# Kernel optimization log

Hardware: AMD Instinct MI355X
Metric: run time of the kernel (lower is better)

Reference implementation:

```python
import jax, jax.numpy as jnp
import numpy as np

N = 4096          # nodes
F_IN = 1386       # txt_feat_len
NHID = 1024       # per-head hidden
NHEADS = 8
CODE = 64         # code_len
LRELU_ALPHA = 0.2
NEG_INF = -9e15


def _build_adj(x):
    # F.normalize + cosine sim, threshold 0.8, sign -> {0,1}, then symmetric D^-1/2 A D^-1/2
    norm = jnp.maximum(jnp.linalg.norm(x, axis=1, keepdims=True), 1e-12)
    xn = x / norm
    sim = xn @ xn.T                                  # (N,N)
    A = (sim >= 0.8).astype(x.dtype)                 # sign after thresholding
    rowsum = A.sum(axis=1)
    r = jnp.where(rowsum > 0, rowsum ** -0.5, 0.0)
    adj = r[:, None] * A * r[None, :]                # symmetric normalized
    return jax.lax.stop_gradient(adj)                # torch code detaches x / adj is non-diff


def _gat_head(x, W, a, adj, concat):
    # x: (N,Fin), W: (Fin,H), a: (2H,1)
    H = W.shape[1]
    Wh = x @ W                                        # (N,H)
    f1 = Wh @ a[:H]                                   # (N,1)
    f2 = Wh @ a[H:]                                   # (N,1)
    e = jax.nn.leaky_relu(f1 + f2.T, LRELU_ALPHA)     # (N,N) pairwise scores
    e = jnp.where(adj > 0, e, NEG_INF)
    att = jax.nn.softmax(e, axis=1)                   # masked softmax (dropout off: eval)
    h = att @ Wh                                      # (N,H)
    return jax.nn.elu(h) if concat else h


def setup_inputs() -> dict:
    key = jax.random.key(0)
    k = jax.random.split(key, 5)
    x = jax.random.normal(k[0], (N, F_IN), dtype=jnp.float32)
    s_in = 1.0 / np.sqrt(F_IN)
    W_att = jax.random.uniform(k[1], (NHEADS, F_IN, NHID), jnp.float32, -s_in, s_in)
    a_att = jax.random.uniform(k[2], (NHEADS, 2 * NHID, 1), jnp.float32, -0.1, 0.1)
    s_h = 1.0 / np.sqrt(NHEADS * NHID)
    W_out = jax.random.uniform(k[3], (NHEADS * NHID, CODE), jnp.float32, -s_h, s_h)
    a_out = jax.random.uniform(k[4], (2 * CODE, 1), jnp.float32, -0.1, 0.1)
    return {"x": x, "W_att": W_att, "a_att": a_att, "W_out": W_out, "a_out": a_out}


def reference(x, W_att, a_att, W_out, a_out):
    adj = _build_adj(x)
    # 8 concat heads, vmapped over the head axis
    heads = jax.vmap(lambda W, a: _gat_head(x, W, a, adj, True))(W_att, a_att)  # (8,N,NHID)
    h = jnp.transpose(heads, (1, 0, 2)).reshape(N, NHEADS * NHID)               # cat dim=1
    out = _gat_head(h, W_out, a_out, adj, False)                                # (N,CODE)
    code = jnp.tanh(1.0 * out)                                                   # alpha=1.0
    return code
```

## Files before the change

kernel.cpp:

```cpp
#include <hip/hip_runtime.h>
#include <hip/hip_bf16.h>
#include <stdint.h>
#include <math.h>


typedef __bf16 bf16x8 __attribute__((ext_vector_type(8)));
typedef float  f32x4  __attribute__((ext_vector_type(4)));
typedef unsigned short ushort8 __attribute__((ext_vector_type(8)));

#define AS1C(p) ((const __attribute__((address_space(1))) void*)(p))
#define AS3(p)  ((__attribute__((address_space(3))) void*)(p))

#define MODE_BF16 0
#define MODE_SIM  1
#define MODE_F32  2

__device__ __forceinline__ float bfbits2f(unsigned short u) {
    return __uint_as_float(((unsigned)u) << 16);
}
__device__ __forceinline__ unsigned short f2bfbits(float v) {
    __hip_bfloat16 b = __float2bfloat16(v);
    return *(unsigned short*)&b;
}

template<int MODE>
__global__ __launch_bounds__(256, 2)
void gemm_bt(const __hip_bfloat16* __restrict__ A,
             const __hip_bfloat16* __restrict__ B,
             int lda, int ldb, int K,
             void* __restrict__ Cv, int ldc, int Nreal,
             const float* __restrict__ norms,
             unsigned* __restrict__ mask,
             unsigned* __restrict__ summary,
             const float* __restrict__ a_att,
             float2* __restrict__ f12,
             int head_base,
             long long zA, long long zB, long long zC)
{
    __shared__ __align__(16) __hip_bfloat16 As[128 * 32];
    __shared__ __align__(16) __hip_bfloat16 Bs[128 * 32];

    const int tid  = threadIdx.x;
    const int lane = tid & 63;
    const int wave = tid >> 6;
    const int z    = blockIdx.z;

    int bx, by;
    if (MODE == MODE_SIM) {
        const int id = blockIdx.x;
        int t = (int)((sqrtf(8.f * id + 1.f) - 1.f) * 0.5f);
        while (t * (t + 1) / 2 > id) --t;
        while ((t + 1) * (t + 2) / 2 <= id) ++t;
        by = t; bx = id - t * (t + 1) / 2;
    } else {
        bx = blockIdx.x; by = blockIdx.y;
    }
    const int m0 = bx * 128;
    const int n0 = by * 128;

    A += (long long)z * zA;
    B += (long long)z * zB;

    f32x4 acc[4][4];
#pragma unroll
    for (int i = 0; i < 4; ++i)
#pragma unroll
        for (int j = 0; j < 4; ++j)
#pragma unroll
            for (int k = 0; k < 4; ++k) acc[i][j][k] = 0.f;

    const int wm = wave >> 1, wn = wave & 1;
    const int q  = lane >> 4, ln = lane & 15;

    const int kIters = K >> 5;
    for (int kt = 0; kt < kIters; ++kt) {
        __syncthreads();
#pragma unroll
        for (int p = 0; p < 2; ++p) {
            const int t   = p * 256 + tid;
            const int row = t >> 2;
            const int kb  = (t & 3) ^ ((t >> 3) & 3);
            const __hip_bfloat16* ga = A + (long long)(m0 + row) * lda + kt * 32 + kb * 8;
            const __hip_bfloat16* gb = B + (long long)(n0 + row) * ldb + kt * 32 + kb * 8;
            __hip_bfloat16* sa = As + (p * 256 + wave * 64) * 8;
            __hip_bfloat16* sb = Bs + (p * 256 + wave * 64) * 8;
            __builtin_amdgcn_global_load_lds(AS1C(ga), AS3(sa), 16, 0, 0);
            __builtin_amdgcn_global_load_lds(AS1C(gb), AS3(sb), 16, 0, 0);
        }
        __syncthreads();

        bf16x8 afr[4], bfr[4];
#pragma unroll
        for (int rg = 0; rg < 4; ++rg) {
            const int r = wm * 64 + rg * 16 + ln;
            const int s = q ^ ((r >> 1) & 3);
            afr[rg] = *(const bf16x8*)(As + r * 32 + s * 8);
        }
#pragma unroll
        for (int cg = 0; cg < 4; ++cg) {
            const int r = wn * 64 + cg * 16 + ln;
            const int s = q ^ ((r >> 1) & 3);
            bfr[cg] = *(const bf16x8*)(Bs + r * 32 + s * 8);
        }
#pragma unroll
        for (int rg = 0; rg < 4; ++rg)
#pragma unroll
            for (int cg = 0; cg < 4; ++cg)
                acc[rg][cg] = __builtin_amdgcn_mfma_f32_16x16x32_bf16(
                    afr[rg], bfr[cg], acc[rg][cg], 0, 0, 0);
    }

    const float* a1 = nullptr; const float* a2 = nullptr;
    if (MODE == MODE_BF16) {
        a1 = a_att + (long long)(head_base + z) * 2048;
        a2 = a1 + 1024;
    }
#pragma unroll
    for (int rg = 0; rg < 4; ++rg) {
#pragma unroll
        for (int i = 0; i < 4; ++i) {
            const int row = m0 + wm * 64 + rg * 16 + q * 4 + i;
            float s1 = 0.f, s2 = 0.f;
#pragma unroll
            for (int cg = 0; cg < 4; ++cg) {
                const int col = n0 + wn * 64 + cg * 16 + ln;
                const float v = acc[rg][cg][i];
                if (MODE == MODE_BF16) {
                    __hip_bfloat16* C = (__hip_bfloat16*)Cv + (long long)z * zC;
                    C[(long long)row * ldc + col] = __float2bfloat16(v);
                    s1 += v * a1[col];
                    s2 += v * a2[col];
                } else if (MODE == MODE_SIM) {
                    if (v >= 0.8f * norms[row] * norms[col]) {
                        atomicOr(&mask[row * 128 + (col >> 5)], 1u << (col & 31));
                        atomicOr(&summary[row * 4 + (col >> 10)], 1u << ((col >> 5) & 31));
                        atomicOr(&mask[col * 128 + (row >> 5)], 1u << (row & 31));
                        atomicOr(&summary[col * 4 + (row >> 10)], 1u << ((row >> 5) & 31));
                    }
                } else {
                    if (col < Nreal) {
                        float* C = (float*)Cv + (long long)z * zC;
                        C[(long long)row * ldc + col] = v;
                    }
                }
            }
            if (MODE == MODE_BF16) {
#pragma unroll
                for (int off = 8; off; off >>= 1) {
                    s1 += __shfl_down(s1, off, 16);
                    s2 += __shfl_down(s2, off, 16);
                }
                if (ln == 0) {
                    float2* fp = f12 + (long long)(head_base + z) * 4096 + row;
                    atomicAdd(&fp->x, s1);
                    atomicAdd(&fp->y, s2);
                }
            }
        }
    }
}

__global__ void convert_x(const float* __restrict__ x,
                          __hip_bfloat16* __restrict__ xb,
                          float* __restrict__ norms)
{
    const int i = blockIdx.x, tid = threadIdx.x;
    float ss = 0.f;
    for (int c = tid; c < 1408; c += 256) {
        float v = (c < 1386) ? x[(long long)i * 1386 + c] : 0.f;
        xb[(long long)i * 1408 + c] = __float2bfloat16(v);
        ss += v * v;
    }
    for (int off = 32; off; off >>= 1) ss += __shfl_down(ss, off);
    __shared__ float red[4];
    if ((tid & 63) == 0) red[tid >> 6] = ss;
    __syncthreads();
    if (tid == 0) norms[i] = fmaxf(sqrtf(red[0] + red[1] + red[2] + red[3]), 1e-12f);
}

__global__ void transpose_bf(const float* __restrict__ src,
                             __hip_bfloat16* __restrict__ dst,
                             int K, int N, int Kpad, int Npad,
                             long long sStride, long long dStride)
{
    __shared__ float ts[32][33];
    const int b  = blockIdx.z;
    const int k0 = blockIdx.x * 32;
    const int n0 = blockIdx.y * 32;
    const int tx = threadIdx.x, ty = threadIdx.y;
    const float* s = src + b * sStride;
    __hip_bfloat16* d = dst + b * dStride;
#pragma unroll
    for (int i = 0; i < 4; ++i) {
        const int k = k0 + ty + i * 8;
        const int n = n0 + tx;
        ts[ty + i * 8][tx] = (k < K && n < N) ? s[(long long)k * N + n] : 0.f;
    }
    __syncthreads();
#pragma unroll
    for (int i = 0; i < 4; ++i) {
        const int n  = n0 + ty + i * 8;
        const int kk = k0 + tx;
        if (n < Npad && kk < Kpad)
            d[(long long)n * Kpad + kk] = __float2bfloat16(ts[tx][ty + i * 8]);
    }
}

__global__ __launch_bounds__(256)
void attn_head(const __hip_bfloat16* __restrict__ Wh,
               const float2* __restrict__ f12,
               const unsigned* __restrict__ mask,
               const unsigned* __restrict__ summary,
               __hip_bfloat16* __restrict__ hout,
               int head_base, int BH)
{
    const int wv   = threadIdx.x >> 6;
    const int lane = threadIdx.x & 63;
    const int i    = blockIdx.x * 4 + wv;
    const int hl   = blockIdx.y;
    const int h    = head_base + hl;
    const float2* f = f12 + (long long)h * 4096;
    const float f1 = f[i].x;
    const unsigned* mrow = mask + (long long)i * 128;
    const __hip_bfloat16* WhH = Wh + (long long)hl * 4096 * 1024;
    const uint4 sm = *(const uint4*)(summary + (long long)i * 4);
    unsigned sw[4] = { sm.x, sm.y, sm.z, sm.w };
    const int cbase = lane * 16;

    float m = -INFINITY, l = 0.f;
    float acc[16];
#pragma unroll
    for (int k = 0; k < 16; ++k) acc[k] = 0.f;

#pragma unroll
    for (int s = 0; s < 4; ++s) {
        unsigned sb = sw[s];
        while (sb) {
            const int w = s * 32 + __builtin_ctz(sb);
            sb &= sb - 1;
            unsigned bits = mrow[w];
            while (bits) {
                const int j = w * 32 + __builtin_ctz(bits);
                bits &= bits - 1;
                float e = f1 + f[j].y;
                e = e > 0.f ? e : 0.2f * e;
                float wgt;
                if (e > m) {
                    const float sc = __expf(m - e);
                    l *= sc;
#pragma unroll
                    for (int k = 0; k < 16; ++k) acc[k] *= sc;
                    m = e; wgt = 1.f;
                } else {
                    wgt = __expf(e - m);
                }
                l += wgt;
                const ushort8* p = (const ushort8*)(WhH + (long long)j * 1024 + cbase);
                const ushort8 w0 = p[0], w1 = p[1];
#pragma unroll
                for (int k = 0; k < 8; ++k) acc[k]     += wgt * bfbits2f(w0[k]);
#pragma unroll
                for (int k = 0; k < 8; ++k) acc[k + 8] += wgt * bfbits2f(w1[k]);
            }
        }
    }
    const float inv = 1.f / l;
    ushort8 o0, o1;
#pragma unroll
    for (int k = 0; k < 8; ++k) {
        float v = acc[k] * inv;     v = v > 0.f ? v : (__expf(v) - 1.f); o0[k] = f2bfbits(v);
        float u = acc[k + 8] * inv; u = u > 0.f ? u : (__expf(u) - 1.f); o1[k] = f2bfbits(u);
    }
    ushort8* op = (ushort8*)(hout + (long long)i * (BH * 1024) + (long long)hl * 1024 + cbase);
    op[0] = o0; op[1] = o1;
}

__global__ void out_reduce_f(const float* __restrict__ parts,
                             const float* __restrict__ a_out,
                             float* __restrict__ Cout,
                             float* __restrict__ f1o,
                             float* __restrict__ f2o)
{
    const int i = blockIdx.x, c = threadIdx.x;
    float v = 0.f;
#pragma unroll
    for (int z = 0; z < 16; ++z) v += parts[(long long)z * 4096 * 64 + (long long)i * 64 + c];
    Cout[(long long)i * 64 + c] = v;
    float s1 = v * a_out[c];
    float s2 = v * a_out[64 + c];
    for (int off = 32; off; off >>= 1) { s1 += __shfl_down(s1, off); s2 += __shfl_down(s2, off); }
    if (c == 0) { f1o[i] = s1; f2o[i] = s2; }
}

__global__ __launch_bounds__(256)
void attn_out(const float* __restrict__ Cout,
              const float* __restrict__ f1o,
              const float* __restrict__ f2o,
              const unsigned* __restrict__ mask,
              const unsigned* __restrict__ summary,
              float* __restrict__ out)
{
    const int wv = threadIdx.x >> 6;
    const int c  = threadIdx.x & 63;
    const int i  = blockIdx.x * 4 + wv;
    const float f1 = f1o[i];
    const unsigned* mrow = mask + (long long)i * 128;
    const uint4 sm = *(const uint4*)(summary + (long long)i * 4);
    unsigned sw[4] = { sm.x, sm.y, sm.z, sm.w };
    float m = -INFINITY, l = 0.f, acc = 0.f;
#pragma unroll
    for (int s = 0; s < 4; ++s) {
        unsigned sb = sw[s];
        while (sb) {
            const int w = s * 32 + __builtin_ctz(sb);
            sb &= sb - 1;
            unsigned bits = mrow[w];
            while (bits) {
                const int j = w * 32 + __builtin_ctz(bits);
                bits &= bits - 1;
                float e = f1 + f2o[j];
                e = e > 0.f ? e : 0.2f * e;
                float wgt;
                if (e > m) { const float sc = __expf(m - e); l *= sc; acc *= sc; m = e; wgt = 1.f; }
                else       { wgt = __expf(e - m); }
                l += wgt;
                acc += wgt * Cout[(long long)j * 64 + c];
            }
        }
    }
    out[(long long)i * 64 + c] = tanhf(acc / l);
}

extern "C" void kernel_launch(void* const* d_in, const int* in_sizes, int n_in,
                              void* d_out, int out_size, void* d_ws, size_t ws_size,
                              hipStream_t stream)
{
    (void)in_sizes; (void)n_in; (void)out_size;
    const float* x     = (const float*)d_in[0];
    const float* W_att = (const float*)d_in[1];
    const float* a_att = (const float*)d_in[2];
    const float* W_out = (const float*)d_in[3];
    const float* a_out = (const float*)d_in[4];
    float* out = (float*)d_out;

    char* ws = (char*)d_ws;
    size_t off = 0;
    auto alloc = [&](size_t bytes) -> void* {
        void* p = ws + off;
        off += (bytes + 255) & ~(size_t)255;
        return p;
    };

    __hip_bfloat16* x_bf  = (__hip_bfloat16*)alloc(4096LL * 1408 * 2);
    __hip_bfloat16* Wt_bf = (__hip_bfloat16*)alloc(8LL * 1024 * 1408 * 2);
    __hip_bfloat16* WoutT = (__hip_bfloat16*)alloc(128LL * 8192 * 2);
    float*          norms = (float*)alloc(4096 * 4);
    unsigned*       mask  = (unsigned*)alloc(4096LL * 128 * 4);
    unsigned*       summ  = (unsigned*)alloc(4096LL * 4 * 4);
    float2*         f12   = (float2*)alloc(8LL * 4096 * 8);
    float*          parts = (float*)alloc(16LL * 4096 * 64 * 4);
    float*          Cout  = (float*)alloc(4096LL * 64 * 4);
    float*          f1o   = (float*)alloc(4096 * 4);
    float*          f2o   = (float*)alloc(4096 * 4);
    const size_t statics = off;

    int BH = 8;
    while (BH > 1 && statics + (size_t)BH * 2 * 8388608ULL + 512 > ws_size) BH >>= 1;
    if (statics + (size_t)BH * 2 * 8388608ULL + 512 > ws_size) return;
    __hip_bfloat16* Wh_b   = (__hip_bfloat16*)alloc((size_t)BH * 4096 * 1024 * 2);
    __hip_bfloat16* hout_b = (__hip_bfloat16*)alloc((size_t)BH * 4096 * 1024 * 2);

    hipMemsetAsync(mask, 0, 4096LL * 128 * 4, stream);
    hipMemsetAsync(summ, 0, 4096LL * 4 * 4, stream);
    hipMemsetAsync(f12,  0, 8LL * 4096 * 8, stream);

    convert_x<<<4096, 256, 0, stream>>>(x, x_bf, norms);
    transpose_bf<<<dim3(44, 32, 8), dim3(32, 8), 0, stream>>>(
        W_att, Wt_bf, 1386, 1024, 1408, 1024, 1386LL * 1024, 1024LL * 1408);
    transpose_bf<<<dim3(256, 4, 1), dim3(32, 8), 0, stream>>>(
        W_out, WoutT, 8192, 64, 8192, 128, 0, 0);

    gemm_bt<MODE_SIM><<<dim3(528, 1, 1), 256, 0, stream>>>(
        x_bf, x_bf, 1408, 1408, 1408, nullptr, 0, 0, norms, mask, summ,
        nullptr, nullptr, 0, 0, 0, 0);

    const int nBatches = 8 / BH;
    for (int bi = 0; bi < nBatches; ++bi) {
        gemm_bt<MODE_BF16><<<dim3(32, 8, BH), 256, 0, stream>>>(
            x_bf, Wt_bf + (long long)bi * BH * 1024 * 1408, 1408, 1408, 1408,
            Wh_b, 1024, 1024, nullptr, nullptr, nullptr,
            a_att, f12, bi * BH,
            0, 1024LL * 1408, 4096LL * 1024);
        attn_head<<<dim3(1024, BH), 256, 0, stream>>>(Wh_b, f12, mask, summ, hout_b, bi * BH, BH);
        gemm_bt<MODE_F32><<<dim3(32, 1, 2 * BH), 256, 0, stream>>>(
            hout_b, WoutT + (long long)bi * BH * 1024, BH * 1024, 8192, 512,
            parts + (long long)bi * 2 * BH * 4096 * 64, 64, 64,
            nullptr, nullptr, nullptr, nullptr, nullptr, 0,
            512, 512, 4096LL * 64);
    }

    out_reduce_f<<<4096, 64, 0, stream>>>(parts, a_out, Cout, f1o, f2o);
    attn_out<<<1024, 256, 0, stream>>>(Cout, f1o, f2o, mask, summ, out);
}
```

Baseline: 349.1 us.

## Fuse prep and GEMM launches, compute attention projections via precomputed W·a

Merges the conversion and transpose kernels into one prestage launch, and merges the similarity GEMM, all eight head GEMMs and the f1/f2 projection into a single mega_gemm launch. The attention scores f1/f2 are now computed algebraically as x·(W·a) in fp32 instead of through atomic reductions in the GEMM epilogue. It also drops the head-batching fallback and always allocates full Wh/hout buffers. The aim is fewer launches, better CU fill and no epilogue atomics, at the cost of extra workspace. f1/f2 now come from fp32 x and W rather than from the bf16 Wh values.

Measured after the change: 326.3 us. 1.07x faster.

```diff
diff --git a/kernel.cpp b/kernel.cpp
--- a/kernel.cpp
+++ b/kernel.cpp
@@ -24,42 +24,22 @@
 }
 
 template<int MODE>
-__global__ __launch_bounds__(256, 2)
-void gemm_bt(const __hip_bfloat16* __restrict__ A,
-             const __hip_bfloat16* __restrict__ B,
-             int lda, int ldb, int K,
-             void* __restrict__ Cv, int ldc, int Nreal,
-             const float* __restrict__ norms,
-             unsigned* __restrict__ mask,
-             unsigned* __restrict__ summary,
-             const float* __restrict__ a_att,
-             float2* __restrict__ f12,
-             int head_base,
-             long long zA, long long zB, long long zC)
-{
-    __shared__ __align__(16) __hip_bfloat16 As[128 * 32];
-    __shared__ __align__(16) __hip_bfloat16 Bs[128 * 32];
-
+__device__ __forceinline__ void gemm_body(
+    __hip_bfloat16* __restrict__ As, __hip_bfloat16* __restrict__ Bs,
+    int bx, int by,
+    const __hip_bfloat16* __restrict__ A,
+    const __hip_bfloat16* __restrict__ B,
+    int lda, int ldb, int K,
+    void* __restrict__ Cv, int ldc, int Nreal,
+    const float* __restrict__ norms,
+    unsigned* __restrict__ mask,
+    unsigned* __restrict__ summary)
+{
     const int tid  = threadIdx.x;
     const int lane = tid & 63;
     const int wave = tid >> 6;
-    const int z    = blockIdx.z;
-
-    int bx, by;
-    if (MODE == MODE_SIM) {
-        const int id = blockIdx.x;
-        int t = (int)((sqrtf(8.f * id + 1.f) - 1.f) * 0.5f);
-        while (t * (t + 1) / 2 > id) --t;
-        while ((t + 1) * (t + 2) / 2 <= id) ++t;
-        by = t; bx = id - t * (t + 1) / 2;
-    } else {
-        bx = blockIdx.x; by = blockIdx.y;
-    }
-    const int m0 = bx * 128;
-    const int n0 = by * 128;
-
-    A += (long long)z * zA;
-    B += (long long)z * zB;
+    const int m0   = bx * 128;
+    const int n0   = by * 128;
 
     f32x4 acc[4][4];
 #pragma unroll
@@ -110,26 +90,18 @@
                     afr[rg], bfr[cg], acc[rg][cg], 0, 0, 0);
     }
 
-    const float* a1 = nullptr; const float* a2 = nullptr;
-    if (MODE == MODE_BF16) {
-        a1 = a_att + (long long)(head_base + z) * 2048;
-        a2 = a1 + 1024;
-    }
 #pragma unroll
     for (int rg = 0; rg < 4; ++rg) {
 #pragma unroll
-        for (int i = 0; i < 4; ++i) {
-            const int row = m0 + wm * 64 + rg * 16 + q * 4 + i;
-            float s1 = 0.f, s2 = 0.f;
-#pragma unroll
-            for (int cg = 0; cg < 4; ++cg) {
+        for (int cg = 0; cg < 4; ++cg) {
+#pragma unroll
+            for (int i = 0; i < 4; ++i) {
+                const int row = m0 + wm * 64 + rg * 16 + q * 4 + i;
                 const int col = n0 + wn * 64 + cg * 16 + ln;
                 const float v = acc[rg][cg][i];
                 if (MODE == MODE_BF16) {
-                    __hip_bfloat16* C = (__hip_bfloat16*)Cv + (long long)z * zC;
+                    __hip_bfloat16* C = (__hip_bfloat16*)Cv;
                     C[(long long)row * ldc + col] = __float2bfloat16(v);
-                    s1 += v * a1[col];
-                    s2 += v * a2[col];
                 } else if (MODE == MODE_SIM) {
                     if (v >= 0.8f * norms[row] * norms[col]) {
                         atomicOr(&mask[row * 128 + (col >> 5)], 1u << (col & 31));
@@ -139,71 +111,177 @@
                     }
                 } else {
                     if (col < Nreal) {
-                        float* C = (float*)Cv + (long long)z * zC;
+                        float* C = (float*)Cv;
                         C[(long long)row * ldc + col] = v;
                     }
                 }
             }
-            if (MODE == MODE_BF16) {
-#pragma unroll
-                for (int off = 8; off; off >>= 1) {
-                    s1 += __shfl_down(s1, off, 16);
-                    s2 += __shfl_down(s2, off, 16);
-                }
-                if (ln == 0) {
-                    float2* fp = f12 + (long long)(head_base + z) * 4096 + row;
-                    atomicAdd(&fp->x, s1);
-                    atomicAdd(&fp->y, s2);
-                }
+        }
+    }
+}
+
+__global__ __launch_bounds__(256)
+void prestage(const float* __restrict__ x,
+              const float* __restrict__ W_att,
+              const float* __restrict__ W_out,
+              const float* __restrict__ a_att,
+              __hip_bfloat16* __restrict__ x_bf,
+              float* __restrict__ norms,
+              __hip_bfloat16* __restrict__ Wt_bf,
+              __hip_bfloat16* __restrict__ WoutT,
+              float* __restrict__ wa)
+{
+    __shared__ float ts[32][33];
+    __shared__ float red[4];
+    const int id  = blockIdx.x;
+    const int tid = threadIdx.x;
+
+    if (id < 4096) {
+        const int i = id;
+        float ss = 0.f;
+        for (int c = tid; c < 1408; c += 256) {
+            float v = (c < 1386) ? x[(long long)i * 1386 + c] : 0.f;
+            x_bf[(long long)i * 1408 + c] = __float2bfloat16(v);
+            ss += v * v;
+        }
+        for (int off = 32; off; off >>= 1) ss += __shfl_down(ss, off);
+        if ((tid & 63) == 0) red[tid >> 6] = ss;
+        __syncthreads();
+        if (tid == 0) norms[i] = fmaxf(sqrtf(red[0] + red[1] + red[2] + red[3]), 1e-12f);
+        return;
+    }
+    if (id < 16384) {
+        const float* s; __hip_bfloat16* d;
+        int K, N, Kpad, Npad, k0, n0;
+        if (id < 15360) {
+            const int b = id - 4096;
+            const int h = b / 1408, r = b % 1408;
+            const int kx = r % 44, ny = r / 44;
+            s = W_att + (long long)h * 1386 * 1024;
+            d = Wt_bf + (long long)h * 1024 * 1408;
+            K = 1386; N = 1024; Kpad = 1408; Npad = 1024;
+            k0 = kx * 32; n0 = ny * 32;
+        } else {
+            const int r = id - 15360;
+            s = W_out; d = WoutT;
+            K = 8192; N = 64; Kpad = 8192; Npad = 128;
+            k0 = (r & 255) * 32; n0 = (r >> 8) * 32;
+        }
+        const int tx = tid & 31, ty = tid >> 5;
+#pragma unroll
+        for (int i = 0; i < 4; ++i) {
+            const int k = k0 + ty + i * 8;
+            const int n = n0 + tx;
+            ts[ty + i * 8][tx] = (k < K && n < N) ? s[(long long)k * N + n] : 0.f;
+        }
+        __syncthreads();
+#pragma unroll
+        for (int i = 0; i < 4; ++i) {
+            const int n  = n0 + ty + i * 8;
+            const int kk = k0 + tx;
+            if (n < Npad && kk < Kpad)
+                d[(long long)n * Kpad + kk] = __float2bfloat16(ts[tx][ty + i * 8]);
+        }
+        return;
+    }
+    {
+        const int b = id - 16384;
+        const int h = b / 352, r = b % 352;
+        const int wave = tid >> 6, lane = tid & 63;
+        const int c = r * 4 + wave;
+        float s1 = 0.f, s2 = 0.f;
+        if (c < 1386) {
+            const float* wr = W_att + ((long long)h * 1386 + c) * 1024;
+            const float* a1 = a_att + (long long)h * 2048;
+            const float* a2 = a1 + 1024;
+#pragma unroll
+            for (int t = 0; t < 16; ++t) {
+                const int j = lane + t * 64;
+                const float w = wr[j];
+                s1 += w * a1[j];
+                s2 += w * a2[j];
             }
         }
-    }
-}
-
-__global__ void convert_x(const float* __restrict__ x,
-                          __hip_bfloat16* __restrict__ xb,
-                          float* __restrict__ norms)
-{
-    const int i = blockIdx.x, tid = threadIdx.x;
-    float ss = 0.f;
-    for (int c = tid; c < 1408; c += 256) {
-        float v = (c < 1386) ? x[(long long)i * 1386 + c] : 0.f;
-        xb[(long long)i * 1408 + c] = __float2bfloat16(v);
-        ss += v * v;
-    }
-    for (int off = 32; off; off >>= 1) ss += __shfl_down(ss, off);
-    __shared__ float red[4];
-    if ((tid & 63) == 0) red[tid >> 6] = ss;
-    __syncthreads();
-    if (tid == 0) norms[i] = fmaxf(sqrtf(red[0] + red[1] + red[2] + red[3]), 1e-12f);
-}
-
-__global__ void transpose_bf(const float* __restrict__ src,
-                             __hip_bfloat16* __restrict__ dst,
-                             int K, int N, int Kpad, int Npad,
-                             long long sStride, long long dStride)
-{
-    __shared__ float ts[32][33];
-    const int b  = blockIdx.z;
-    const int k0 = blockIdx.x * 32;
-    const int n0 = blockIdx.y * 32;
-    const int tx = threadIdx.x, ty = threadIdx.y;
-    const float* s = src + b * sStride;
-    __hip_bfloat16* d = dst + b * dStride;
-#pragma unroll
-    for (int i = 0; i < 4; ++i) {
-        const int k = k0 + ty + i * 8;
-        const int n = n0 + tx;
-        ts[ty + i * 8][tx] = (k < K && n < N) ? s[(long long)k * N + n] : 0.f;
-    }
-    __syncthreads();
-#pragma unroll
-    for (int i = 0; i < 4; ++i) {
-        const int n  = n0 + ty + i * 8;
-        const int kk = k0 + tx;
-        if (n < Npad && kk < Kpad)
-            d[(long long)n * Kpad + kk] = __float2bfloat16(ts[tx][ty + i * 8]);
-    }
+        for (int off = 32; off; off >>= 1) { s1 += __shfl_down(s1, off); s2 += __shfl_down(s2, off); }
+        if (lane == 0) {
+            wa[(h * 2 + 0) * 1408 + c] = s1;
+            wa[(h * 2 + 1) * 1408 + c] = s2;
+        }
+    }
+}
+
+__global__ __launch_bounds__(256, 2)
+void mega_gemm(const __hip_bfloat16* __restrict__ x_bf,
+               const __hip_bfloat16* __restrict__ Wt_bf,
+               __hip_bfloat16* __restrict__ Wh,
+               const float* __restrict__ norms,
+               unsigned* __restrict__ mask,
+               unsigned* __restrict__ summ,
+               const float* __restrict__ x,
+               const float* __restrict__ wa,
+               float2* __restrict__ f12)
+{
+    __shared__ __align__(16) __hip_bfloat16 As[128 * 32];
+    __shared__ __align__(16) __hip_bfloat16 Bs[128 * 32];
+    const int id = blockIdx.x;
+
+    if (id < 528) {
+        int t = (int)((sqrtf(8.f * id + 1.f) - 1.f) * 0.5f);
+        while (t * (t + 1) / 2 > id) --t;
+        while ((t + 1) * (t + 2) / 2 <= id) ++t;
+        const int by = t, bx = id - t * (t + 1) / 2;
+        gemm_body<MODE_SIM>(As, Bs, bx, by, x_bf, x_bf, 1408, 1408, 1408,
+                            nullptr, 0, 0, norms, mask, summ);
+        return;
+    }
+    if (id < 2576) {
+        const int b  = id - 528;
+        const int z  = b >> 8;
+        const int r  = b & 255;
+        const int bx = r & 31, by = r >> 5;
+        gemm_body<MODE_BF16>(As, Bs, bx, by,
+                             x_bf, Wt_bf + (long long)z * 1024 * 1408,
+                             1408, 1408, 1408,
+                             Wh + (long long)z * 4096 * 1024, 1024, 1024,
+                             nullptr, nullptr, nullptr);
+        return;
+    }
+    {
+        const int b    = id - 2576;
+        const int wave = threadIdx.x >> 6, lane = threadIdx.x & 63;
+        const int i    = b * 4 + wave;
+        float s[16];
+#pragma unroll
+        for (int j = 0; j < 16; ++j) s[j] = 0.f;
+        const float* xr = x + (long long)i * 1386;
+        for (int c = lane; c < 1386; c += 64) {
+            const float v = xr[c];
+#pragma unroll
+            for (int j = 0; j < 16; ++j) s[j] += v * wa[j * 1408 + c];
+        }
+#pragma unroll
+        for (int j = 0; j < 16; ++j)
+            for (int off = 32; off; off >>= 1) s[j] += __shfl_down(s[j], off);
+        if (lane == 0) {
+#pragma unroll
+            for (int h = 0; h < 8; ++h)
+                f12[(long long)h * 4096 + i] = make_float2(s[h * 2], s[h * 2 + 1]);
+        }
+    }
+}
+
+__global__ __launch_bounds__(256, 2)
+void out_gemm(const __hip_bfloat16* __restrict__ hout,
+              const __hip_bfloat16* __restrict__ WoutT,
+              float* __restrict__ parts)
+{
+    __shared__ __align__(16) __hip_bfloat16 As[128 * 32];
+    __shared__ __align__(16) __hip_bfloat16 Bs[128 * 32];
+    const int z = blockIdx.z;
+    gemm_body<MODE_F32>(As, Bs, blockIdx.x, 0,
+                        hout + z * 512, WoutT + z * 512, 8192, 8192, 512,
+                        parts + (long long)z * 4096 * 64, 64, 64,
+                        nullptr, nullptr, nullptr);
 }
 
 __global__ __launch_bounds__(256)
@@ -211,18 +289,16 @@
                const float2* __restrict__ f12,
                const unsigned* __restrict__ mask,
                const unsigned* __restrict__ summary,
-               __hip_bfloat16* __restrict__ hout,
-               int head_base, int BH)
+               __hip_bfloat16* __restrict__ hout)
 {
     const int wv   = threadIdx.x >> 6;
     const int lane = threadIdx.x & 63;
     const int i    = blockIdx.x * 4 + wv;
-    const int hl   = blockIdx.y;
-    const int h    = head_base + hl;
+    const int h    = blockIdx.y;
     const float2* f = f12 + (long long)h * 4096;
     const float f1 = f[i].x;
     const unsigned* mrow = mask + (long long)i * 128;
-    const __hip_bfloat16* WhH = Wh + (long long)hl * 4096 * 1024;
+    const __hip_bfloat16* WhH = Wh + (long long)h * 4096 * 1024;
     const uint4 sm = *(const uint4*)(summary + (long long)i * 4);
     unsigned sw[4] = { sm.x, sm.y, sm.z, sm.w };
     const int cbase = lane * 16;
@@ -271,7 +347,7 @@
         float v = acc[k] * inv;     v = v > 0.f ? v : (__expf(v) - 1.f); o0[k] = f2bfbits(v);
         float u = acc[k + 8] * inv; u = u > 0.f ? u : (__expf(u) - 1.f); o1[k] = f2bfbits(u);
     }
-    ushort8* op = (ushort8*)(hout + (long long)i * (BH * 1024) + (long long)hl * 1024 + cbase);
+    ushort8* op = (ushort8*)(hout + (long long)i * 8192 + (long long)h * 1024 + cbase);
     op[0] = o0; op[1] = o1;
 }
 
@@ -357,47 +433,27 @@
     float*          norms = (float*)alloc(4096 * 4);
     unsigned*       mask  = (unsigned*)alloc(4096LL * 128 * 4);
     unsigned*       summ  = (unsigned*)alloc(4096LL * 4 * 4);
+    float*          wa    = (float*)alloc(16LL * 1408 * 4);
     float2*         f12   = (float2*)alloc(8LL * 4096 * 8);
     float*          parts = (float*)alloc(16LL * 4096 * 64 * 4);
     float*          Cout  = (float*)alloc(4096LL * 64 * 4);
     float*          f1o   = (float*)alloc(4096 * 4);
     float*          f2o   = (float*)alloc(4096 * 4);
-    const size_t statics = off;
-
-    int BH = 8;
-    while (BH > 1 && statics + (size_t)BH * 2 * 8388608ULL + 512 > ws_size) BH >>= 1;
-    if (statics + (size_t)BH * 2 * 8388608ULL + 512 > ws_size) return;
-    __hip_bfloat16* Wh_b   = (__hip_bfloat16*)alloc((size_t)BH * 4096 * 1024 * 2);
-    __hip_bfloat16* hout_b = (__hip_bfloat16*)alloc((size_t)BH * 4096 * 1024 * 2);
-
-    hipMemsetAsync(mask, 0, 4096LL * 128 * 4, stream);
-    hipMemsetAsync(summ, 0, 4096LL * 4 * 4, stream);
-    hipMemsetAsync(f12,  0, 8LL * 4096 * 8, stream);
-
-    convert_x<<<4096, 256, 0, stream>>>(x, x_bf, norms);
-    transpose_bf<<<dim3(44, 32, 8), dim3(32, 8), 0, stream>>>(
-        W_att, Wt_bf, 1386, 1024, 1408, 1024, 1386LL * 1024, 1024LL * 1408);
-    transpose_bf<<<dim3(256, 4, 1), dim3(32, 8), 0, stream>>>(
-        W_out, WoutT, 8192, 64, 8192, 128, 0, 0);
-
-    gemm_bt<MODE_SIM><<<dim3(528, 1, 1), 256, 0, stream>>>(
-        x_bf, x_bf, 1408, 1408, 1408, nullptr, 0, 0, norms, mask, summ,
-        nullptr, nullptr, 0, 0, 0, 0);
-
-    const int nBatches = 8 / BH;
-    for (int bi = 0; bi < nBatches; ++bi) {
-        gemm_bt<MODE_BF16><<<dim3(32, 8, BH), 256, 0, stream>>>(
-            x_bf, Wt_bf + (long long)bi * BH * 1024 * 1408, 1408, 1408, 1408,
-            Wh_b, 1024, 1024, nullptr, nullptr, nullptr,
-            a_att, f12, bi * BH,
-            0, 1024LL * 1408, 4096LL * 1024);
-        attn_head<<<dim3(1024, BH), 256, 0, stream>>>(Wh_b, f12, mask, summ, hout_b, bi * BH, BH);
-        gemm_bt<MODE_F32><<<dim3(32, 1, 2 * BH), 256, 0, stream>>>(
-            hout_b, WoutT + (long long)bi * BH * 1024, BH * 1024, 8192, 512,
-            parts + (long long)bi * 2 * BH * 4096 * 64, 64, 64,
-            nullptr, nullptr, nullptr, nullptr, nullptr, 0,
-            512, 512, 4096LL * 64);
-    }
+    __hip_bfloat16* Wh    = (__hip_bfloat16*)alloc(8LL * 4096 * 1024 * 2);
+    __hip_bfloat16* hout  = (__hip_bfloat16*)alloc(8LL * 4096 * 1024 * 2);
+    if (off > ws_size) return;
+
+    hipMemsetAsync(mask, 0, 4096LL * 128 * 4 + 4096LL * 4 * 4, stream);
+
+    prestage<<<19200, 256, 0, stream>>>(x, W_att, W_out, a_att,
+                                        x_bf, norms, Wt_bf, WoutT, wa);
+
+    mega_gemm<<<3600, 256, 0, stream>>>(x_bf, Wt_bf, Wh, norms, mask, summ,
+                                        x, wa, f12);
+
+    attn_head<<<dim3(1024, 8), 256, 0, stream>>>(Wh, f12, mask, summ, hout);
+
+    out_gemm<<<dim3(32, 1, 16), 256, 0, stream>>>(hout, WoutT, parts);
 
     out_reduce_f<<<4096, 64, 0, stream>>>(parts, a_out, Cout, f1o, f2o);
     attn_out<<<1024, 256, 0, stream>>>(Cout, f1o, f2o, mask, summ, out);
```
